# Kernel tuning notes

Measured on AMD Instinct MI355X. Metric: run time of the kernel, lower is better.

The kernel has to match this reference:

```python
import jax, jax.numpy as jnp
import numpy as np
import math

B, C, H, W = 8, 256, 64, 64
CQK = C // 8

def _conv1x1(x, w, b):
    # x: [B,C,H,W], w: [O,C], b: [O]  (1x1 conv == per-pixel linear)
    return jnp.einsum('bchw,oc->bohw', x, w) + b[None, :, None, None]

def setup_inputs() -> dict:
    key = jax.random.key(0)
    ks = jax.random.split(key, 7)
    inputs = jax.random.normal(ks[0], (B, C, H, W), dtype=jnp.float32)
    # init_weight: normal(0, sqrt(2/(k*k*out_channels))) for 1x1 convs
    wq = jax.random.normal(ks[1], (CQK, C), dtype=jnp.float32) * math.sqrt(2.0 / CQK)
    wk = jax.random.normal(ks[2], (CQK, C), dtype=jnp.float32) * math.sqrt(2.0 / CQK)
    wv = jax.random.normal(ks[3], (C, C), dtype=jnp.float32) * math.sqrt(2.0 / C)
    bq = jnp.zeros((CQK,), dtype=jnp.float32)
    bk = jnp.zeros((CQK,), dtype=jnp.float32)
    bv = jnp.zeros((C,), dtype=jnp.float32)
    # torch init is zeros(1); use nonzero so the attention path contributes
    alpha = jnp.full((1,), 0.5, dtype=jnp.float32)
    return {"inputs": inputs, "wq": wq, "bq": bq, "wk": wk, "bk": bk,
            "wv": wv, "bv": bv, "alpha": alpha}

def reference(inputs, wq, bq, wk, bk, wv, bv, alpha):
    b, c, h, w = inputs.shape
    n = h * w
    q = _conv1x1(inputs, wq, bq).reshape(b, -1, n)          # [B, C/8, N]
    k = _conv1x1(inputs, wk, bk).reshape(b, -1, n)          # [B, C/8, N]
    v = _conv1x1(inputs, wv, bv).reshape(b, c, n)           # [B, C, N]
    # attention_weight[b, i, j] = q[:, i] . k[:, j]
    attn = jnp.einsum('bdi,bdj->bij', q, k)                 # [B, N, N]
    attn = jax.nn.softmax(attn, axis=-1)
    # value @ attn^T : out[b, c, i] = sum_j v[b, c, j] * attn[b, i, j]
    out = jnp.einsum('bcj,bij->bci', v, attn)               # [B, C, N]
    return alpha[0] * out.reshape(inputs.shape) + inputs
```

## Files before the change

kernel.cpp:

```cpp
#include <hip/hip_runtime.h>
#include <math.h>

#define B_  8
#define C_  256
#define N_  4096
#define NJC (N_ / 128)
#define PLD 136

using frag  = __attribute__((ext_vector_type(8))) short;
using f32x4 = __attribute__((ext_vector_type(4))) float;

__device__ __forceinline__ unsigned short f2bf(float f) {
    unsigned u = __float_as_uint(f);
    u += 0x7fffu + ((u >> 16) & 1u);
    return (unsigned short)(u >> 16);
}
__device__ __forceinline__ float bf2f(unsigned short h) {
    return __uint_as_float(((unsigned)h) << 16);
}
#define PK2(a, b) (((unsigned)(a)) | (((unsigned)(b)) << 16))

__device__ __forceinline__ f32x4 fmax4(f32x4 a, f32x4 b) {
    f32x4 r;
    r[0] = fmaxf(a[0], b[0]); r[1] = fmaxf(a[1], b[1]);
    r[2] = fmaxf(a[2], b[2]); r[3] = fmaxf(a[3], b[3]);
    return r;
}

__global__ __launch_bounds__(256) void wprep_kernel(
    const float* __restrict__ wq, const float* __restrict__ wk,
    const float* __restrict__ wv,
    unsigned short* __restrict__ whf, unsigned short* __restrict__ wlf)
{
    const int fid  = blockIdx.x * 256 + threadIdx.x;
    if (fid >= 20 * 8 * 64) return;
    const int g    = fid >> 9;
    const int kc   = (fid >> 6) & 7;
    const int lane = fid & 63;
    const int r16  = lane & 15, q = lane >> 4;

    const float* src; int row;
    if (g < 2)      { src = wq; row = g * 16 + r16; }
    else if (g < 4) { src = wk; row = (g - 2) * 16 + r16; }
    else            { src = wv; row = (g - 4) * 16 + r16; }

    const float* wp = src + row * 256 + kc * 32 + q * 8;
    float v[8];
#pragma unroll
    for (int j = 0; j < 8; ++j) v[j] = wp[j];

    unsigned short h[8];
#pragma unroll
    for (int j = 0; j < 8; ++j) h[j] = f2bf(v[j]);
    uint4 U;
    U.x = PK2(h[0], h[1]); U.y = PK2(h[2], h[3]);
    U.z = PK2(h[4], h[5]); U.w = PK2(h[6], h[7]);
    *(uint4*)&whf[(size_t)fid * 8] = U;

    if (g < 4) {
        unsigned short l[8];
#pragma unroll
        for (int j = 0; j < 8; ++j) l[j] = f2bf(v[j] - bf2f(h[j]));
        uint4 V;
        V.x = PK2(l[0], l[1]); V.y = PK2(l[2], l[3]);
        V.z = PK2(l[4], l[5]); V.w = PK2(l[6], l[7]);
        *(uint4*)&wlf[(size_t)fid * 8] = V;
    }
}

__global__ __launch_bounds__(256, 2) void proj_kernel(
    const float* __restrict__ x,
    const float* __restrict__ bq, const float* __restrict__ bk,
    const float* __restrict__ bv,
    const unsigned short* __restrict__ whf, const unsigned short* __restrict__ wlf,
    unsigned short* __restrict__ qh, unsigned short* __restrict__ ql,
    unsigned short* __restrict__ kh, unsigned short* __restrict__ kl,
    unsigned short* __restrict__ vbf)
{
    __shared__ unsigned xpk[64 * 260 + 4];

    const int tid  = threadIdx.x;
    const int w    = tid >> 6;
    const int lane = tid & 63;
    const int quad = lane >> 4;
    const int l16  = lane & 15;
    const int n0   = blockIdx.x * 64;
    const int b    = blockIdx.y;

    {
        const int p  = tid & 63;
        const int cb = tid >> 6;
        const float* xbase = x + (size_t)b * C_ * N_ + n0 + p;
#pragma unroll 16
        for (int s = 0; s < 64; ++s) {
            const int c = s * 4 + cb;
            const float v = xbase[(size_t)c * N_];
            const unsigned short hb = f2bf(v);
            const unsigned short lb = f2bf(v - bf2f(hb));
            xpk[p * 260 + c] = (((unsigned)hb) << 16) | lb;
        }
    }
    __syncthreads();

    const frag* wh = (const frag*)whf;
    const frag* wl = (const frag*)wlf;
    const int n = n0 + w * 16 + l16;

    f32x4 acc[20];
#pragma unroll
    for (int g = 0; g < 20; ++g) acc[g] = (f32x4){0.f, 0.f, 0.f, 0.f};

    for (int kc = 0; kc < 8; ++kc) {
        const unsigned* row = &xpk[(w * 16 + l16) * 260 + kc * 32 + quad * 8];
        const uint4 A  = *(const uint4*)row;
        const uint4 Bv = *(const uint4*)(row + 4);
        frag bh, bl;
        unsigned* bhp = (unsigned*)&bh;
        unsigned* blp = (unsigned*)&bl;
        bhp[0] = __builtin_amdgcn_perm(A.y,  A.x,  0x07060302u);
        bhp[1] = __builtin_amdgcn_perm(A.w,  A.z,  0x07060302u);
        bhp[2] = __builtin_amdgcn_perm(Bv.y, Bv.x, 0x07060302u);
        bhp[3] = __builtin_amdgcn_perm(Bv.w, Bv.z, 0x07060302u);
        blp[0] = __builtin_amdgcn_perm(A.y,  A.x,  0x05040100u);
        blp[1] = __builtin_amdgcn_perm(A.w,  A.z,  0x05040100u);
        blp[2] = __builtin_amdgcn_perm(Bv.y, Bv.x, 0x05040100u);
        blp[3] = __builtin_amdgcn_perm(Bv.w, Bv.z, 0x05040100u);

#pragma unroll
        for (int g = 0; g < 4; ++g) {
            const frag ah = wh[(g * 8 + kc) * 64 + lane];
            const frag al = wl[(g * 8 + kc) * 64 + lane];
            acc[g] = __builtin_amdgcn_mfma_f32_16x16x32_bf16(ah, bh, acc[g], 0, 0, 0);
            acc[g] = __builtin_amdgcn_mfma_f32_16x16x32_bf16(al, bh, acc[g], 0, 0, 0);
            acc[g] = __builtin_amdgcn_mfma_f32_16x16x32_bf16(ah, bl, acc[g], 0, 0, 0);
        }
#pragma unroll
        for (int g = 4; g < 20; ++g) {
            const frag ah = wh[(g * 8 + kc) * 64 + lane];
            acc[g] = __builtin_amdgcn_mfma_f32_16x16x32_bf16(ah, bh, acc[g], 0, 0, 0);
        }
    }

#pragma unroll
    for (int g = 0; g < 4; ++g) {
        const bool isq = (g < 2);
        const float* bias = isq ? bq : bk;
        const int dbase = (isq ? g : g - 2) * 16 + quad * 4;
        unsigned short hs[4], ls[4];
#pragma unroll
        for (int r = 0; r < 4; ++r) {
            const float f = acc[g][r] + bias[dbase + r];
            hs[r] = f2bf(f);
            ls[r] = f2bf(f - bf2f(hs[r]));
        }
        const size_t off = ((size_t)(b * N_ + n)) * 32 + dbase;
        *(uint2*)&(isq ? qh : kh)[off] = make_uint2(PK2(hs[0], hs[1]), PK2(hs[2], hs[3]));
        *(uint2*)&(isq ? ql : kl)[off] = make_uint2(PK2(ls[0], ls[1]), PK2(ls[2], ls[3]));
    }
#pragma unroll
    for (int g = 4; g < 20; ++g) {
#pragma unroll
        for (int r = 0; r < 4; ++r) {
            const int c = (g - 4) * 16 + quad * 4 + r;
            vbf[((size_t)b * C_ + c) * N_ + n] = f2bf(acc[g][r] + bv[c]);
        }
    }
}

__global__ __launch_bounds__(512, 2) void attn_kernel(
    const unsigned short* __restrict__ qh, const unsigned short* __restrict__ ql,
    const unsigned short* __restrict__ khg, const unsigned short* __restrict__ klg,
    const unsigned short* __restrict__ vbf,
    const float* __restrict__ x, const float* __restrict__ alpha_p,
    float* __restrict__ out)
{
    __shared__ __align__(16) short kbuf[2][2][128 * 32];
    __shared__ __align__(16) short p_s[2][128 * PLD];
    __shared__ float alpha_s[2][128];
    __shared__ float l_s[128];

    const int tid  = threadIdx.x;
    const int w    = tid >> 6;
    const int lane = tid & 63;
    const int quad = lane >> 4;
    const int l16  = lane & 15;
    const int b    = blockIdx.y;
    const int i0   = blockIdx.x * 128;

    const size_t qoff = ((size_t)(b * N_ + i0 + w * 16 + l16)) * 32 + quad * 8;
    const frag qhf = *(const frag*)(qh + qoff);
    const frag qlf = *(const frag*)(ql + qoff);

    const unsigned short* khb = khg + (size_t)b * N_ * 32;
    const unsigned short* klb = klg + (size_t)b * N_ * 32;
    const unsigned short* vb  = vbf + (size_t)b * C_ * N_;

    f32x4 o[8][2];
#pragma unroll
    for (int it = 0; it < 8; ++it) {
        o[it][0] = (f32x4){0.f, 0.f, 0.f, 0.f};
        o[it][1] = (f32x4){0.f, 0.f, 0.f, 0.f};
    }

    float m_run = -INFINITY, l_run = 0.f;

    const int r_st  = w * 16 + l16;
    const int qc_st = quad;
    const int gsto  = r_st * 32 + qc_st * 8;
    const int lsto  = qc_st * 1024 + r_st * 8;

    {
        const uint4 h0 = *(const uint4*)(khb + gsto);
        const uint4 l0 = *(const uint4*)(klb + gsto);
        *(uint4*)&kbuf[0][0][lsto] = h0;
        *(uint4*)&kbuf[0][1][lsto] = l0;
    }
    __syncthreads();

    for (int jc = 0; jc < NJC; ++jc) {
        const int bf = jc & 1;

        f32x4 st[8];
#pragma unroll
        for (int js = 0; js < 8; ++js) {
            const frag ka  = *(const frag*)&kbuf[bf][0][quad * 1024 + (js * 16 + l16) * 8];
            const frag kb2 = *(const frag*)&kbuf[bf][1][quad * 1024 + (js * 16 + l16) * 8];
            f32x4 s = (f32x4){0.f, 0.f, 0.f, 0.f};
            s = __builtin_amdgcn_mfma_f32_16x16x32_bf16(ka, qhf, s, 0, 0, 0);
            s = __builtin_amdgcn_mfma_f32_16x16x32_bf16(ka, qlf, s, 0, 0, 0);
            s = __builtin_amdgcn_mfma_f32_16x16x32_bf16(kb2, qhf, s, 0, 0, 0);
            st[js] = s;
        }

        const int jn = (jc + 1 < NJC) ? jc + 1 : jc;
        const uint4 knh = *(const uint4*)(khb + (size_t)jn * 4096 + gsto);
        const uint4 knl = *(const uint4*)(klb + (size_t)jn * 4096 + gsto);

        frag vf[4][2];
#pragma unroll
        for (int ks = 0; ks < 4; ++ks)
#pragma unroll
            for (int ct = 0; ct < 2; ++ct)
                vf[ks][ct] = *(const frag*)(vb
                    + (size_t)(w * 32 + ct * 16 + l16) * N_
                    + jc * 128 + ks * 32 + quad * 8);

        f32x4 t0 = fmax4(fmax4(st[0], st[1]), fmax4(st[2], st[3]));
        f32x4 t1 = fmax4(fmax4(st[4], st[5]), fmax4(st[6], st[7]));
        t0 = fmax4(t0, t1);
        float mx = fmaxf(fmaxf(t0[0], t0[1]), fmaxf(t0[2], t0[3]));
        mx = fmaxf(mx, __shfl_xor(mx, 16));
        mx = fmaxf(mx, __shfl_xor(mx, 32));
        const float mnew = fmaxf(m_run, mx);
        const float sc   = __expf(m_run - mnew);

        f32x4 ps4 = (f32x4){0.f, 0.f, 0.f, 0.f};
#pragma unroll
        for (int js = 0; js < 8; ++js) {
#pragma unroll
            for (int r = 0; r < 4; ++r) st[js][r] = __expf(st[js][r] - mnew);
            ps4[0] += st[js][0]; ps4[1] += st[js][1];
            ps4[2] += st[js][2]; ps4[3] += st[js][3];
        }
        float ps = (ps4[0] + ps4[1]) + (ps4[2] + ps4[3]);
        ps += __shfl_xor(ps, 16);
        ps += __shfl_xor(ps, 32);
        l_run = l_run * sc + ps;
        m_run = mnew;
        if (quad == 0) alpha_s[bf][w * 16 + l16] = sc;

#pragma unroll
        for (int js = 0; js < 8; ++js) {
            const unsigned a0 = __float_as_uint(st[js][0]) + 0x8000u;
            const unsigned a1 = __float_as_uint(st[js][1]) + 0x8000u;
            const unsigned a2 = __float_as_uint(st[js][2]) + 0x8000u;
            const unsigned a3 = __float_as_uint(st[js][3]) + 0x8000u;
            const unsigned p01 = __builtin_amdgcn_perm(a1, a0, 0x07060302u);
            const unsigned p23 = __builtin_amdgcn_perm(a3, a2, 0x07060302u);
            *(uint2*)&p_s[bf][(w * 16 + l16) * PLD + js * 16 + quad * 4] =
                make_uint2(p01, p23);
        }

        *(uint4*)&kbuf[bf ^ 1][0][lsto] = knh;
        *(uint4*)&kbuf[bf ^ 1][1][lsto] = knl;

        __syncthreads();

#pragma unroll
        for (int it = 0; it < 8; ++it)
#pragma unroll
            for (int r = 0; r < 4; ++r) {
                const float al = alpha_s[bf][it * 16 + quad * 4 + r];
                o[it][0][r] *= al;
                o[it][1][r] *= al;
            }

#pragma unroll
        for (int ks = 0; ks < 4; ++ks) {
#pragma unroll
            for (int it = 0; it < 8; ++it) {
                const frag pf = *(const frag*)&p_s[bf][(it * 16 + l16) * PLD
                                                       + ks * 32 + quad * 8];
                o[it][0] = __builtin_amdgcn_mfma_f32_16x16x32_bf16(pf, vf[ks][0], o[it][0], 0, 0, 0);
                o[it][1] = __builtin_amdgcn_mfma_f32_16x16x32_bf16(pf, vf[ks][1], o[it][1], 0, 0, 0);
            }
        }
    }

    if (quad == 0) l_s[w * 16 + l16] = l_run;
    __syncthreads();
    const float av = alpha_p[0];

#pragma unroll
    for (int it = 0; it < 8; ++it) {
        float invl[4];
#pragma unroll
        for (int r = 0; r < 4; ++r) invl[r] = 1.f / l_s[it * 16 + quad * 4 + r];
#pragma unroll
        for (int ct = 0; ct < 2; ++ct) {
            const int c = w * 32 + ct * 16 + l16;
            const size_t base = (size_t)b * C_ * N_ + (size_t)c * N_
                                + i0 + it * 16 + quad * 4;
            const float4 xv = *(const float4*)(x + base);
            float4 ov;
            ov.x = av * (o[it][ct][0] * invl[0]) + xv.x;
            ov.y = av * (o[it][ct][1] * invl[1]) + xv.y;
            ov.z = av * (o[it][ct][2] * invl[2]) + xv.z;
            ov.w = av * (o[it][ct][3] * invl[3]) + xv.w;
            *(float4*)(out + base) = ov;
        }
    }
}

extern "C" void kernel_launch(void* const* d_in, const int* in_sizes, int n_in,
                              void* d_out, int out_size, void* d_ws, size_t ws_size,
                              hipStream_t stream)
{
    const float* x  = (const float*)d_in[0];
    const float* wq = (const float*)d_in[1];
    const float* bq = (const float*)d_in[2];
    const float* wk = (const float*)d_in[3];
    const float* bk = (const float*)d_in[4];
    const float* wv = (const float*)d_in[5];
    const float* bv = (const float*)d_in[6];
    const float* al = (const float*)d_in[7];
    float* out = (float*)d_out;

    char* ws = (char*)d_ws;
    unsigned short* qh  = (unsigned short*)(ws + 0);
    unsigned short* ql  = (unsigned short*)(ws + (size_t)2  * 1024 * 1024);
    unsigned short* kh  = (unsigned short*)(ws + (size_t)4  * 1024 * 1024);
    unsigned short* kl  = (unsigned short*)(ws + (size_t)6  * 1024 * 1024);
    unsigned short* vbf = (unsigned short*)(ws + (size_t)8  * 1024 * 1024);
    unsigned short* whf = (unsigned short*)(ws + (size_t)24 * 1024 * 1024);
    unsigned short* wlf = (unsigned short*)(ws + (size_t)24 * 1024 * 1024 + 256 * 1024);

    wprep_kernel<<<40, 256, 0, stream>>>(wq, wk, wv, whf, wlf);
    proj_kernel<<<dim3(N_ / 64, B_), 256, 0, stream>>>(
        x, bq, bk, bv, whf, wlf, qh, ql, kh, kl, vbf);
    attn_kernel<<<dim3(N_ / 128, B_), 512, 0, stream>>>(
        qh, ql, kh, kl, vbf, x, al, out);
}
```

Baseline: 216.0 us.

## Shrink attention tile to 64 queries per block and fold log2e into Q

```diff
diff --git a/kernel.cpp b/kernel.cpp
--- a/kernel.cpp
+++ b/kernel.cpp
@@ -6,6 +6,7 @@
 #define N_  4096
 #define NJC (N_ / 128)
 #define PLD 136
+#define LOG2E 1.4426950408889634f
 
 using frag  = __attribute__((ext_vector_type(8))) short;
 using f32x4 = __attribute__((ext_vector_type(4))) float;
@@ -24,6 +25,12 @@
     f32x4 r;
     r[0] = fmaxf(a[0], b[0]); r[1] = fmaxf(a[1], b[1]);
     r[2] = fmaxf(a[2], b[2]); r[3] = fmaxf(a[3], b[3]);
+    return r;
+}
+
+__device__ __forceinline__ float exp2_raw(float x) {
+    float r;
+    asm("v_exp_f32 %0, %1" : "=v"(r) : "v"(x));
     return r;
 }
 
@@ -44,10 +51,11 @@
     else if (g < 4) { src = wk; row = (g - 2) * 16 + r16; }
     else            { src = wv; row = (g - 4) * 16 + r16; }
 
+    const float scl = (g < 2) ? LOG2E : 1.0f;
     const float* wp = src + row * 256 + kc * 32 + q * 8;
     float v[8];
 #pragma unroll
-    for (int j = 0; j < 8; ++j) v[j] = wp[j];
+    for (int j = 0; j < 8; ++j) v[j] = wp[j] * scl;
 
     unsigned short h[8];
 #pragma unroll
@@ -145,11 +153,12 @@
     for (int g = 0; g < 4; ++g) {
         const bool isq = (g < 2);
         const float* bias = isq ? bq : bk;
+        const float bscl = isq ? LOG2E : 1.0f;
         const int dbase = (isq ? g : g - 2) * 16 + quad * 4;
         unsigned short hs[4], ls[4];
 #pragma unroll
         for (int r = 0; r < 4; ++r) {
-            const float f = acc[g][r] + bias[dbase + r];
+            const float f = acc[g][r] + bias[dbase + r] * bscl;
             hs[r] = f2bf(f);
             ls[r] = f2bf(f - bf2f(hs[r]));
         }
@@ -167,7 +176,7 @@
     }
 }
 
-__global__ __launch_bounds__(512, 2) void attn_kernel(
+__global__ __launch_bounds__(256, 2) void attn_kernel(
     const unsigned short* __restrict__ qh, const unsigned short* __restrict__ ql,
     const unsigned short* __restrict__ khg, const unsigned short* __restrict__ klg,
     const unsigned short* __restrict__ vbf,
@@ -175,9 +184,9 @@
     float* __restrict__ out)
 {
     __shared__ __align__(16) short kbuf[2][2][128 * 32];
-    __shared__ __align__(16) short p_s[2][128 * PLD];
-    __shared__ float alpha_s[2][128];
-    __shared__ float l_s[128];
+    __shared__ __align__(16) short p_s[2][64 * PLD];
+    __shared__ float alpha_s[2][64];
+    __shared__ float l_s[64];
 
     const int tid  = threadIdx.x;
     const int w    = tid >> 6;
@@ -185,7 +194,7 @@
     const int quad = lane >> 4;
     const int l16  = lane & 15;
     const int b    = blockIdx.y;
-    const int i0   = blockIdx.x * 128;
+    const int i0   = blockIdx.x * 64;
 
     const size_t qoff = ((size_t)(b * N_ + i0 + w * 16 + l16)) * 32 + quad * 8;
     const frag qhf = *(const frag*)(qh + qoff);
@@ -195,25 +204,29 @@
     const unsigned short* klb = klg + (size_t)b * N_ * 32;
     const unsigned short* vb  = vbf + (size_t)b * C_ * N_;
 
-    f32x4 o[8][2];
-#pragma unroll
-    for (int it = 0; it < 8; ++it) {
-        o[it][0] = (f32x4){0.f, 0.f, 0.f, 0.f};
-        o[it][1] = (f32x4){0.f, 0.f, 0.f, 0.f};
-    }
+    f32x4 o[4][4];
+#pragma unroll
+    for (int it = 0; it < 4; ++it)
+#pragma unroll
+        for (int ct = 0; ct < 4; ++ct)
+            o[it][ct] = (f32x4){0.f, 0.f, 0.f, 0.f};
 
     float m_run = -INFINITY, l_run = 0.f;
 
-    const int r_st  = w * 16 + l16;
-    const int qc_st = quad;
-    const int gsto  = r_st * 32 + qc_st * 8;
-    const int lsto  = qc_st * 1024 + r_st * 8;
+    const int ch0 = tid, ch1 = tid + 256;
+    const int g0 = ch0 * 8, g1 = ch1 * 8;
+    const int s0 = (ch0 & 3) * 1024 + (ch0 >> 2) * 8;
+    const int s1 = (ch1 & 3) * 1024 + (ch1 >> 2) * 8;
 
     {
-        const uint4 h0 = *(const uint4*)(khb + gsto);
-        const uint4 l0 = *(const uint4*)(klb + gsto);
-        *(uint4*)&kbuf[0][0][lsto] = h0;
-        *(uint4*)&kbuf[0][1][lsto] = l0;
+        const uint4 h0 = *(const uint4*)(khb + g0);
+        const uint4 h1 = *(const uint4*)(khb + g1);
+        const uint4 l0 = *(const uint4*)(klb + g0);
+        const uint4 l1 = *(const uint4*)(klb + g1);
+        *(uint4*)&kbuf[0][0][s0] = h0;
+        *(uint4*)&kbuf[0][0][s1] = h1;
+        *(uint4*)&kbuf[0][1][s0] = l0;
+        *(uint4*)&kbuf[0][1][s1] = l1;
     }
     __syncthreads();
 
@@ -233,16 +246,18 @@
         }
 
         const int jn = (jc + 1 < NJC) ? jc + 1 : jc;
-        const uint4 knh = *(const uint4*)(khb + (size_t)jn * 4096 + gsto);
-        const uint4 knl = *(const uint4*)(klb + (size_t)jn * 4096 + gsto);
-
-        frag vf[4][2];
+        const uint4 knh0 = *(const uint4*)(khb + (size_t)jn * 4096 + g0);
+        const uint4 knh1 = *(const uint4*)(khb + (size_t)jn * 4096 + g1);
+        const uint4 knl0 = *(const uint4*)(klb + (size_t)jn * 4096 + g0);
+        const uint4 knl1 = *(const uint4*)(klb + (size_t)jn * 4096 + g1);
+
+        frag vf[4][4];
 #pragma unroll
         for (int ks = 0; ks < 4; ++ks)
 #pragma unroll
-            for (int ct = 0; ct < 2; ++ct)
+            for (int ct = 0; ct < 4; ++ct)
                 vf[ks][ct] = *(const frag*)(vb
-                    + (size_t)(w * 32 + ct * 16 + l16) * N_
+                    + (size_t)(w * 64 + ct * 16 + l16) * N_
                     + jc * 128 + ks * 32 + quad * 8);
 
         f32x4 t0 = fmax4(fmax4(st[0], st[1]), fmax4(st[2], st[3]));
@@ -252,13 +267,13 @@
         mx = fmaxf(mx, __shfl_xor(mx, 16));
         mx = fmaxf(mx, __shfl_xor(mx, 32));
         const float mnew = fmaxf(m_run, mx);
-        const float sc   = __expf(m_run - mnew);
+        const float sc   = exp2_raw(m_run - mnew);
 
         f32x4 ps4 = (f32x4){0.f, 0.f, 0.f, 0.f};
 #pragma unroll
         for (int js = 0; js < 8; ++js) {
 #pragma unroll
-            for (int r = 0; r < 4; ++r) st[js][r] = __expf(st[js][r] - mnew);
+            for (int r = 0; r < 4; ++r) st[js][r] = exp2_raw(st[js][r] - mnew);
             ps4[0] += st[js][0]; ps4[1] += st[js][1];
             ps4[2] += st[js][2]; ps4[3] += st[js][3];
         }
@@ -281,28 +296,32 @@
                 make_uint2(p01, p23);
         }
 
-        *(uint4*)&kbuf[bf ^ 1][0][lsto] = knh;
-        *(uint4*)&kbuf[bf ^ 1][1][lsto] = knl;
+        *(uint4*)&kbuf[bf ^ 1][0][s0] = knh0;
+        *(uint4*)&kbuf[bf ^ 1][0][s1] = knh1;
+        *(uint4*)&kbuf[bf ^ 1][1][s0] = knl0;
+        *(uint4*)&kbuf[bf ^ 1][1][s1] = knl1;
 
         __syncthreads();
 
 #pragma unroll
-        for (int it = 0; it < 8; ++it)
+        for (int it = 0; it < 4; ++it)
 #pragma unroll
             for (int r = 0; r < 4; ++r) {
                 const float al = alpha_s[bf][it * 16 + quad * 4 + r];
-                o[it][0][r] *= al;
-                o[it][1][r] *= al;
+#pragma unroll
+                for (int ct = 0; ct < 4; ++ct) o[it][ct][r] *= al;
             }
 
 #pragma unroll
         for (int ks = 0; ks < 4; ++ks) {
 #pragma unroll
-            for (int it = 0; it < 8; ++it) {
+            for (int it = 0; it < 4; ++it) {
                 const frag pf = *(const frag*)&p_s[bf][(it * 16 + l16) * PLD
                                                        + ks * 32 + quad * 8];
-                o[it][0] = __builtin_amdgcn_mfma_f32_16x16x32_bf16(pf, vf[ks][0], o[it][0], 0, 0, 0);
-                o[it][1] = __builtin_amdgcn_mfma_f32_16x16x32_bf16(pf, vf[ks][1], o[it][1], 0, 0, 0);
+#pragma unroll
+                for (int ct = 0; ct < 4; ++ct)
+                    o[it][ct] = __builtin_amdgcn_mfma_f32_16x16x32_bf16(
+                        pf, vf[ks][ct], o[it][ct], 0, 0, 0);
             }
         }
     }
@@ -312,13 +331,13 @@
     const float av = alpha_p[0];
 
 #pragma unroll
-    for (int it = 0; it < 8; ++it) {
+    for (int it = 0; it < 4; ++it) {
         float invl[4];
 #pragma unroll
         for (int r = 0; r < 4; ++r) invl[r] = 1.f / l_s[it * 16 + quad * 4 + r];
 #pragma unroll
-        for (int ct = 0; ct < 2; ++ct) {
-            const int c = w * 32 + ct * 16 + l16;
+        for (int ct = 0; ct < 4; ++ct) {
+            const int c = w * 64 + ct * 16 + l16;
             const size_t base = (size_t)b * C_ * N_ + (size_t)c * N_
                                 + i0 + it * 16 + quad * 4;
             const float4 xv = *(const float4*)(x + base);
@@ -358,6 +377,6 @@
     wprep_kernel<<<40, 256, 0, stream>>>(wq, wk, wv, whf, wlf);
     proj_kernel<<<dim3(N_ / 64, B_), 256, 0, stream>>>(
         x, bq, bk, bv, whf, wlf, qh, ql, kh, kl, vbf);
-    attn_kernel<<<dim3(N_ / 128, B_), 512, 0, stream>>>(
+    attn_kernel<<<dim3(N_ / 64, B_), 256, 0, stream>>>(
         qh, ql, kh, kl, vbf, x, al, out);
 }
```

Result: slower. 256.6 us (+18.8%).

## Software-pipeline PV MMA of previous chunk with QK of current chunk; use exp2

Applied to the files above, without the earlier changes.

```diff
diff --git a/kernel.cpp b/kernel.cpp
--- a/kernel.cpp
+++ b/kernel.cpp
@@ -6,6 +6,7 @@
 #define N_  4096
 #define NJC (N_ / 128)
 #define PLD 136
+#define LOG2E 1.4426950408889634f
 
 using frag  = __attribute__((ext_vector_type(8))) short;
 using f32x4 = __attribute__((ext_vector_type(4))) float;
@@ -24,6 +25,12 @@
     f32x4 r;
     r[0] = fmaxf(a[0], b[0]); r[1] = fmaxf(a[1], b[1]);
     r[2] = fmaxf(a[2], b[2]); r[3] = fmaxf(a[3], b[3]);
+    return r;
+}
+
+__device__ __forceinline__ float exp2_raw(float x) {
+    float r;
+    asm("v_exp_f32 %0, %1" : "=v"(r) : "v"(x));
     return r;
 }
 
@@ -44,10 +51,11 @@
     else if (g < 4) { src = wk; row = (g - 2) * 16 + r16; }
     else            { src = wv; row = (g - 4) * 16 + r16; }
 
+    const float scl = (g < 2) ? LOG2E : 1.0f;
     const float* wp = src + row * 256 + kc * 32 + q * 8;
     float v[8];
 #pragma unroll
-    for (int j = 0; j < 8; ++j) v[j] = wp[j];
+    for (int j = 0; j < 8; ++j) v[j] = wp[j] * scl;
 
     unsigned short h[8];
 #pragma unroll
@@ -145,11 +153,12 @@
     for (int g = 0; g < 4; ++g) {
         const bool isq = (g < 2);
         const float* bias = isq ? bq : bk;
+        const float bscl = isq ? LOG2E : 1.0f;
         const int dbase = (isq ? g : g - 2) * 16 + quad * 4;
         unsigned short hs[4], ls[4];
 #pragma unroll
         for (int r = 0; r < 4; ++r) {
-            const float f = acc[g][r] + bias[dbase + r];
+            const float f = acc[g][r] + bias[dbase + r] * bscl;
             hs[r] = f2bf(f);
             ls[r] = f2bf(f - bf2f(hs[r]));
         }
@@ -209,6 +218,8 @@
     const int gsto  = r_st * 32 + qc_st * 8;
     const int lsto  = qc_st * 1024 + r_st * 8;
 
+    frag vf[4][2];
+
     {
         const uint4 h0 = *(const uint4*)(khb + gsto);
         const uint4 l0 = *(const uint4*)(klb + gsto);
@@ -236,7 +247,27 @@
         const uint4 knh = *(const uint4*)(khb + (size_t)jn * 4096 + gsto);
         const uint4 knl = *(const uint4*)(klb + (size_t)jn * 4096 + gsto);
 
-        frag vf[4][2];
+        if (jc > 0) {
+#pragma unroll
+            for (int it = 0; it < 8; ++it)
+#pragma unroll
+                for (int r = 0; r < 4; ++r) {
+                    const float al = alpha_s[bf ^ 1][it * 16 + quad * 4 + r];
+                    o[it][0][r] *= al;
+                    o[it][1][r] *= al;
+                }
+#pragma unroll
+            for (int ks = 0; ks < 4; ++ks) {
+#pragma unroll
+                for (int it = 0; it < 8; ++it) {
+                    const frag pf = *(const frag*)&p_s[bf ^ 1][(it * 16 + l16) * PLD
+                                                              + ks * 32 + quad * 8];
+                    o[it][0] = __builtin_amdgcn_mfma_f32_16x16x32_bf16(pf, vf[ks][0], o[it][0], 0, 0, 0);
+                    o[it][1] = __builtin_amdgcn_mfma_f32_16x16x32_bf16(pf, vf[ks][1], o[it][1], 0, 0, 0);
+                }
+            }
+        }
+
 #pragma unroll
         for (int ks = 0; ks < 4; ++ks)
 #pragma unroll
@@ -252,13 +283,13 @@
         mx = fmaxf(mx, __shfl_xor(mx, 16));
         mx = fmaxf(mx, __shfl_xor(mx, 32));
         const float mnew = fmaxf(m_run, mx);
-        const float sc   = __expf(m_run - mnew);
+        const float sc   = exp2_raw(m_run - mnew);
 
         f32x4 ps4 = (f32x4){0.f, 0.f, 0.f, 0.f};
 #pragma unroll
         for (int js = 0; js < 8; ++js) {
 #pragma unroll
-            for (int r = 0; r < 4; ++r) st[js][r] = __expf(st[js][r] - mnew);
+            for (int r = 0; r < 4; ++r) st[js][r] = exp2_raw(st[js][r] - mnew);
             ps4[0] += st[js][0]; ps4[1] += st[js][1];
             ps4[2] += st[js][2]; ps4[3] += st[js][3];
         }
@@ -285,21 +316,23 @@
         *(uint4*)&kbuf[bf ^ 1][1][lsto] = knl;
 
         __syncthreads();
-
+    }
+
+    {
+        const int bl = (NJC - 1) & 1;
 #pragma unroll
         for (int it = 0; it < 8; ++it)
 #pragma unroll
             for (int r = 0; r < 4; ++r) {
-                const float al = alpha_s[bf][it * 16 + quad * 4 + r];
+                const float al = alpha_s[bl][it * 16 + quad * 4 + r];
                 o[it][0][r] *= al;
                 o[it][1][r] *= al;
             }
-
 #pragma unroll
         for (int ks = 0; ks < 4; ++ks) {
 #pragma unroll
             for (int it = 0; it < 8; ++it) {
-                const frag pf = *(const frag*)&p_s[bf][(it * 16 + l16) * PLD
+                const frag pf = *(const frag*)&p_s[bl][(it * 16 + l16) * PLD
                                                        + ks * 32 + quad * 8];
                 o[it][0] = __builtin_amdgcn_mfma_f32_16x16x32_bf16(pf, vf[ks][0], o[it][0], 0, 0, 0);
                 o[it][1] = __builtin_amdgcn_mfma_f32_16x16x32_bf16(pf, vf[ks][1], o[it][1], 0, 0, 0);
```

New measurement: 215.2 us. No clear change (-0.3%).
